# Kernel optimization log

Hardware: AMD Instinct MI355X
Metric: run time of the kernel (lower is better)

Reference implementation:

```python
import jax, jax.numpy as jnp
import numpy as np

D_MODEL = 2048
N_HEADS = 16
N_KV_HEADS = 4
HEAD_DIM = D_MODEL // N_HEADS  # 128
ROPE_DIM = 128
ROPE_BASE = 10000.0
B, T = 2, 8192


def setup_inputs() -> dict:
    key = jax.random.key(0)
    k1, k2, k3, k4 = jax.random.split(key, 4)
    s = 0.02
    return {
        "x": jax.random.normal(k1, (B, T, D_MODEL), dtype=jnp.float32),
        "wq": jax.random.normal(k2, (N_HEADS * HEAD_DIM, D_MODEL), dtype=jnp.float32) * s,
        "wk": jax.random.normal(k3, (N_KV_HEADS * HEAD_DIM, D_MODEL), dtype=jnp.float32) * s,
        "wv": jax.random.normal(k4, (N_KV_HEADS * HEAD_DIM, D_MODEL), dtype=jnp.float32) * s,
        "pos_offset": 0,
    }


def _shape_heads(y, n_heads):
    b, t, _ = y.shape
    # (B,T,H*D) -> (B,H,T,D)
    return y.reshape(b, t, n_heads, HEAD_DIM).transpose(0, 2, 1, 3)


def _rope(xh, pos_offset):
    # xh: (B,H,T,Dh); rotate first ROPE_DIM dims, llama-style rotate_half.
    t = xh.shape[2]
    half = ROPE_DIM // 2
    inv_freq = 1.0 / (ROPE_BASE ** (jnp.arange(0, ROPE_DIM, 2, dtype=jnp.float32) / ROPE_DIM))  # (half,)
    pos = jnp.arange(t, dtype=jnp.float32) + pos_offset  # (T,)
    freqs = pos[:, None] * inv_freq[None, :]  # (T, half)
    emb = jnp.concatenate([freqs, freqs], axis=-1)  # (T, ROPE_DIM)
    cos = jnp.cos(emb)[None, None]  # (1,1,T,ROPE_DIM)
    sin = jnp.sin(emb)[None, None]
    xr = xh[..., :ROPE_DIM]
    xp = xh[..., ROPE_DIM:]
    rot = jnp.concatenate([-xr[..., half:], xr[..., :half]], axis=-1)
    xr = xr * cos + rot * sin
    return jnp.concatenate([xr, xp], axis=-1) if xp.shape[-1] else xr


def reference(x, wq, wk, wv, pos_offset):
    # torch nn.Linear: y = x @ W.T
    q = jnp.einsum('btd,od->bto', x, wq)
    k = jnp.einsum('btd,od->bto', x, wk)
    v = jnp.einsum('btd,od->bto', x, wv)
    qh = _rope(_shape_heads(q, N_HEADS), pos_offset)    # (B,H,T,Dh)
    kh = _rope(_shape_heads(k, N_KV_HEADS), pos_offset)  # (B,Hkv,T,Dh)
    vh = _shape_heads(v, N_KV_HEADS)                     # (B,Hkv,T,Dh)
    return qh, kh, vh
```

## Files before the change

kernel.cpp:

```cpp
#include <hip/hip_runtime.h>
#include <hip/hip_bf16.h>


typedef __attribute__((ext_vector_type(8))) short short8;
typedef __attribute__((ext_vector_type(4))) float f32x4;

#define Q_BLOCK  33554432u
#define V_BASE   41943040u

__device__ __forceinline__ unsigned short f2bf(float f) {
  unsigned u = __float_as_uint(f);
  u += 0x7FFFu + ((u >> 16) & 1u);
  return (unsigned short)(u >> 16);
}
__device__ __forceinline__ float bf2f(unsigned short h) {
  return __uint_as_float(((unsigned)h) << 16);
}

__global__ void prep_kernel(const float* __restrict__ x,
                            const float* __restrict__ wq,
                            const float* __restrict__ wk,
                            const float* __restrict__ wv,
                            const int* __restrict__ pos_off,
                            unsigned short* __restrict__ Ahi,
                            unsigned short* __restrict__ Alo,
                            unsigned short* __restrict__ Bhi,
                            unsigned short* __restrict__ Blo,
                            float2* __restrict__ rt) {
  const int bid = blockIdx.x, t = threadIdx.x;
  if (bid < 2048) {
    int base = bid * 4096 + t;
    #pragma unroll
    for (int i = 0; i < 16; ++i) {
      int idx = base + i * 256;
      float4 v = ((const float4*)x)[idx];
      ushort4 h, l;
      h.x = f2bf(v.x); l.x = f2bf(v.x - bf2f(h.x));
      h.y = f2bf(v.y); l.y = f2bf(v.y - bf2f(h.y));
      h.z = f2bf(v.z); l.z = f2bf(v.z - bf2f(h.z));
      h.w = f2bf(v.w); l.w = f2bf(v.w - bf2f(h.w));
      ((ushort4*)Ahi)[idx] = h;
      ((ushort4*)Alo)[idx] = l;
    }
  } else if (bid < 2560) {
    int base = (bid - 2048) * 3072 + t;
    #pragma unroll
    for (int i = 0; i < 12; ++i) {
      int idx = base + i * 256;
      int n = idx >> 9, k4 = idx & 511;
      const float* src;
      if (n < 2048)      src = wq + (size_t)n * 2048;
      else if (n < 2560) src = wk + (size_t)(n - 2048) * 2048;
      else               src = wv + (size_t)(n - 2560) * 2048;
      float4 v = ((const float4*)src)[k4];
      ushort4 h, l;
      h.x = f2bf(v.x); l.x = f2bf(v.x - bf2f(h.x));
      h.y = f2bf(v.y); l.y = f2bf(v.y - bf2f(h.y));
      h.z = f2bf(v.z); l.z = f2bf(v.z - bf2f(h.z));
      h.w = f2bf(v.w); l.w = f2bf(v.w - bf2f(h.w));
      ((ushort4*)Bhi)[idx] = h;
      ((ushort4*)Blo)[idx] = l;
    }
  } else {
    __shared__ float sinv[64];
    if (t < 64) sinv[t] = (float)pow(10000.0, -(double)t / 64.0);
    __syncthreads();
    const int po = pos_off[0];
    int base = (bid - 2560) * 4096 + t;
    #pragma unroll
    for (int i = 0; i < 16; ++i) {
      int idx = base + i * 256;
      int trow = idx >> 6, j = idx & 63;
      float ang = (float)(trow + po) * sinv[j];
      double a = (double)ang;
      double k = rint(a * 0.15915494309189535);
      double r = a - k * 6.283185307179586;
      float rf = (float)r;
      rt[idx] = make_float2(cosf(rf), sinf(rf));
    }
  }
}

__global__ __launch_bounds__(512, 2) void gemm8_kernel(
    const unsigned short* __restrict__ Ahi, const unsigned short* __restrict__ Alo,
    const unsigned short* __restrict__ Bhi, const unsigned short* __restrict__ Blo,
    const float2* __restrict__ rt, float* __restrict__ out) {
  __shared__ __align__(16) unsigned short smem[65536];

  const int tid  = threadIdx.x;
  const int lane = tid & 63;
  const int wave = tid >> 6;
  const int wr   = wave >> 2;
  const int wc   = wave & 3;
  const int l15  = lane & 15, lk = lane >> 4;

  const int xcd = blockIdx.x & 7;
  const int loc = blockIdx.x >> 3;
  const int bm = xcd * 8 + loc / 12;
  const int bn = loc % 12;
  const int rowA = bm * 256;
  const int rowB = bn * 256;

  int grow[2], gk[2];
  #pragma unroll
  for (int L = 0; L < 2; ++L) {
    const int o = L * 4096 + tid * 8;
    const int lr = o >> 6;
    const int cs = (o >> 3) & 7;
    const int cl = cs ^ (lr & 7);
    grow[L] = lr + ((cl >> 2) << 7);
    gk[L]   = (cl & 3) << 3;
  }

  const int csA = ((wr << 2) + lk) ^ (l15 & 7);
  const int csB = (((wc >> 1) << 2) + lk) ^ (l15 & 7);

  f32x4 acc[8][4];
  #pragma unroll
  for (int m = 0; m < 8; ++m)
    #pragma unroll
    for (int n = 0; n < 4; ++n)
      acc[m][n] = (f32x4){0.f, 0.f, 0.f, 0.f};

  auto STAGE = [&](int n) {
    const unsigned short* As = (n < 128) ? Ahi : Alo;
    const unsigned short* Bs = (n < 64 || n >= 128) ? Bhi : Blo;
    const int kcol = (n & 63) << 5;
    const int sb = (n & 3) << 14;
    #pragma unroll
    for (int L = 0; L < 2; ++L) {
      const int o = L * 4096 + tid * 8;
      const unsigned short* ga = As + (size_t)(rowA + grow[L]) * 2048 + kcol + gk[L];
      __builtin_amdgcn_global_load_lds(
          (const __attribute__((address_space(1))) void*)ga,
          (__attribute__((address_space(3))) void*)&smem[sb + o], 16, 0, 0);
      const unsigned short* gb = Bs + (size_t)(rowB + grow[L]) * 2048 + kcol + gk[L];
      __builtin_amdgcn_global_load_lds(
          (const __attribute__((address_space(1))) void*)gb,
          (__attribute__((address_space(3))) void*)&smem[sb + 8192 + o], 16, 0, 0);
    }
  };

  STAGE(0); STAGE(1); STAGE(2);

  for (int j = 0; j < 192; ++j) {
    if (j) __builtin_amdgcn_s_barrier();
    if (j + 3 < 192) STAGE(j + 3);
    if (j < 189)       asm volatile("s_waitcnt vmcnt(12)" ::: "memory");
    else if (j == 189) asm volatile("s_waitcnt vmcnt(8)"  ::: "memory");
    else if (j == 190) asm volatile("s_waitcnt vmcnt(4)"  ::: "memory");
    else               asm volatile("s_waitcnt vmcnt(0)"  ::: "memory");
    __builtin_amdgcn_s_barrier();

    const int sb = (j & 3) << 14;
    short8 af[8], bf[4];
    #pragma unroll
    for (int mi = 0; mi < 8; ++mi)
      af[mi] = *(const short8*)&smem[sb + (mi * 16 + l15) * 64 + csA * 8];
    #pragma unroll
    for (int ni = 0; ni < 4; ++ni) {
      const int br = (wc & 1) * 32 + (ni & 1) * 16 + ((ni >> 1) << 6) + l15;
      bf[ni] = *(const short8*)&smem[sb + 8192 + br * 64 + csB * 8];
    }
    __builtin_amdgcn_s_setprio(1);
    #pragma unroll
    for (int mi = 0; mi < 8; ++mi)
      #pragma unroll
      for (int ni = 0; ni < 4; ++ni)
        acc[mi][ni] = __builtin_amdgcn_mfma_f32_16x16x32_bf16(
            af[mi], bf[ni], acc[mi][ni], 0, 0, 0);
    __builtin_amdgcn_s_setprio(0);
  }

  const int headglob = bn * 2 + (wc >> 1);
  size_t base; int nheads, head; bool dorope;
  if (headglob < 16)      { base = 0;       head = headglob;      nheads = 16; dorope = true; }
  else if (headglob < 20) { base = Q_BLOCK; head = headglob - 16; nheads = 4;  dorope = true; }
  else                    { base = V_BASE;  head = headglob - 20; nheads = 4;  dorope = false; }
  const int dbase = (wc & 1) * 32;

  #pragma unroll
  for (int m = 0; m < 8; ++m) {
    #pragma unroll
    for (int r = 0; r < 4; ++r) {
      const int row = bm * 256 + wr * 128 + m * 16 + lk * 4 + r;
      const int b = row >> 13, trow = row & 8191;
      float* op = out + base + (((size_t)(b * nheads + head) * 8192 + trow) << 7);
      #pragma unroll
      for (int n0 = 0; n0 < 2; ++n0) {
        const int d1 = dbase + n0 * 16 + l15;
        const float c1 = acc[m][n0][r];
        const float c2 = acc[m][n0 + 2][r];
        if (dorope) {
          const float2 cs = rt[(trow << 6) + d1];
          op[d1]      = c1 * cs.x - c2 * cs.y;
          op[d1 + 64] = c2 * cs.x + c1 * cs.y;
        } else {
          op[d1]      = c1;
          op[d1 + 64] = c2;
        }
      }
    }
  }
}

__global__ void fallback_kernel(const float* __restrict__ x,
                                const float* __restrict__ wq,
                                const float* __restrict__ wk,
                                const float* __restrict__ wv,
                                const int* __restrict__ pos_off,
                                float* __restrict__ out) {
  __shared__ float xs[2048];
  const int m = blockIdx.x;
  const int b = m >> 13, t = m & 8191;
  const float* xr = x + (size_t)m * 2048;
  for (int i = threadIdx.x; i < 2048; i += 256) xs[i] = xr[i];
  __syncthreads();

  const int n = blockIdx.y * 256 + threadIdx.x;
  const int d = n & 63;
  const float* w; size_t base; int head, nh; bool dorope;
  if (n < 1024)      { head = n >> 6;          w = wq + (size_t)(head * 128 + d) * 2048; base = 0;       nh = 16; dorope = true; }
  else if (n < 1280) { head = (n - 1024) >> 6; w = wk + (size_t)(head * 128 + d) * 2048; base = Q_BLOCK; nh = 4;  dorope = true; }
  else               { head = (n - 1280) >> 6; w = wv + (size_t)(head * 128 + d) * 2048; base = V_BASE;  nh = 4;  dorope = false; }

  const float* w2 = w + 64 * 2048;
  float c1 = 0.f, c2 = 0.f;
  for (int k = 0; k < 2048; ++k) { c1 += xs[k] * w[k]; c2 += xs[k] * w2[k]; }

  float* op = out + base + (((size_t)(b * nh + head) * 8192 + t) << 7);
  if (dorope) {
    double invf = pow(10000.0, -(double)d / 64.0);
    float ang = (float)(t + pos_off[0]) * (float)invf;
    float cs = (float)cos((double)ang), sn = (float)sin((double)ang);
    op[d]      = c1 * cs - c2 * sn;
    op[d + 64] = c2 * cs + c1 * sn;
  } else {
    op[d]      = c1;
    op[d + 64] = c2;
  }
}

extern "C" void kernel_launch(void* const* d_in, const int* in_sizes, int n_in,
                              void* d_out, int out_size, void* d_ws, size_t ws_size,
                              hipStream_t stream) {
  const float* x  = (const float*)d_in[0];
  const float* wq = (const float*)d_in[1];
  const float* wk = (const float*)d_in[2];
  const float* wv = (const float*)d_in[3];
  const int* pos  = (const int*)d_in[4];
  float* out = (float*)d_out;

  const size_t WS_NEEDED = 134217728ull + 25165824ull + 4194304ull;
  if (ws_size < WS_NEEDED) {
    fallback_kernel<<<dim3(16384, 6), 256, 0, stream>>>(x, wq, wk, wv, pos, out);
    return;
  }

  unsigned short* Ahi = (unsigned short*)d_ws;
  unsigned short* Alo = Ahi + 33554432;
  unsigned short* Bhi = Alo + 33554432;
  unsigned short* Blo = Bhi + 6291456;
  float2* rt = (float2*)(Blo + 6291456);

  prep_kernel<<<2688, 256, 0, stream>>>(x, wq, wk, wv, pos,
                                        Ahi, Alo, Bhi, Blo, rt);
  gemm8_kernel<<<768, 512, 0, stream>>>(Ahi, Alo, Bhi, Blo, rt, out);
}
```

Baseline: 922.0 us.

## Restructure GEMM mainloop into 8-wave ping-pong schedule with K=64 tiles

Replaces the 4-stage K=32 buffered loop with a double-buffered K=64 loop. Each iteration is split into four quadrant phases, each separated by barriers, and the global-to-LDS loads for the next tiles are interleaved between MFMA clusters. The LDS layout changes from a half-tile-swizzled K=32 arrangement to a plain 64-column XOR swizzle, with matching fragment offsets. The aim is to hide LDS read and global load latency behind MFMA work, at the cost of many more barriers per iteration and tighter vmcnt/lgkmcnt bookkeeping.

```diff
diff --git a/kernel.cpp b/kernel.cpp
--- a/kernel.cpp
+++ b/kernel.cpp
@@ -108,12 +108,12 @@
     const int lr = o >> 6;
     const int cs = (o >> 3) & 7;
     const int cl = cs ^ (lr & 7);
-    grow[L] = lr + ((cl >> 2) << 7);
-    gk[L]   = (cl & 3) << 3;
-  }
-
-  const int csA = ((wr << 2) + lk) ^ (l15 & 7);
-  const int csB = (((wc >> 1) << 2) + lk) ^ (l15 & 7);
+    grow[L] = lr;
+    gk[L]   = cl << 3;
+  }
+
+  const int ck0 = (((0 << 2) + lk) ^ (l15 & 7)) << 3;
+  const int ck1 = (((1 << 2) + lk) ^ (l15 & 7)) << 3;
 
   f32x4 acc[8][4];
   #pragma unroll
@@ -122,54 +122,123 @@
     for (int n = 0; n < 4; ++n)
       acc[m][n] = (f32x4){0.f, 0.f, 0.f, 0.f};
 
-  auto STAGE = [&](int n) {
-    const unsigned short* As = (n < 128) ? Ahi : Alo;
-    const unsigned short* Bs = (n < 64 || n >= 128) ? Bhi : Blo;
-    const int kcol = (n & 63) << 5;
-    const int sb = (n & 3) << 14;
+  auto Asel = [&](int tt) { return (tt < 64) ? Ahi : Alo; };
+  auto Bsel = [&](int tt) { return (tt < 32 || tt >= 64) ? Bhi : Blo; };
+
+  auto STAGE = [&](int dst, const unsigned short* src, int rowbase, int kc) {
     #pragma unroll
     for (int L = 0; L < 2; ++L) {
       const int o = L * 4096 + tid * 8;
-      const unsigned short* ga = As + (size_t)(rowA + grow[L]) * 2048 + kcol + gk[L];
+      const unsigned short* g = src + (size_t)(rowbase + grow[L]) * 2048 + kc + gk[L];
       __builtin_amdgcn_global_load_lds(
-          (const __attribute__((address_space(1))) void*)ga,
-          (__attribute__((address_space(3))) void*)&smem[sb + o], 16, 0, 0);
-      const unsigned short* gb = Bs + (size_t)(rowB + grow[L]) * 2048 + kcol + gk[L];
-      __builtin_amdgcn_global_load_lds(
-          (const __attribute__((address_space(1))) void*)gb,
-          (__attribute__((address_space(3))) void*)&smem[sb + 8192 + o], 16, 0, 0);
+          (const __attribute__((address_space(1))) void*)g,
+          (__attribute__((address_space(3))) void*)&smem[dst + o], 16, 0, 0);
     }
   };
 
-  STAGE(0); STAGE(1); STAGE(2);
-
-  for (int j = 0; j < 192; ++j) {
-    if (j) __builtin_amdgcn_s_barrier();
-    if (j + 3 < 192) STAGE(j + 3);
-    if (j < 189)       asm volatile("s_waitcnt vmcnt(12)" ::: "memory");
-    else if (j == 189) asm volatile("s_waitcnt vmcnt(8)"  ::: "memory");
-    else if (j == 190) asm volatile("s_waitcnt vmcnt(4)"  ::: "memory");
-    else               asm volatile("s_waitcnt vmcnt(0)"  ::: "memory");
-    __builtin_amdgcn_s_barrier();
-
-    const int sb = (j & 3) << 14;
-    short8 af[8], bf[4];
-    #pragma unroll
-    for (int mi = 0; mi < 8; ++mi)
-      af[mi] = *(const short8*)&smem[sb + (mi * 16 + l15) * 64 + csA * 8];
-    #pragma unroll
-    for (int ni = 0; ni < 4; ++ni) {
-      const int br = (wc & 1) * 32 + (ni & 1) * 16 + ((ni >> 1) << 6) + l15;
-      bf[ni] = *(const short8*)&smem[sb + 8192 + br * 64 + csB * 8];
-    }
+  STAGE(0 + 16384,     Bhi, rowB,       0);
+  STAGE(0 + 24576,     Bhi, rowB + 128, 0);
+  STAGE(0 + 0,         Ahi, rowA,       0);
+  STAGE(0 + 8192,      Ahi, rowA + 128, 0);
+  STAGE(32768 + 16384, Bhi, rowB,       64);
+  STAGE(32768 + 24576, Bhi, rowB + 128, 64);
+  asm volatile("s_waitcnt vmcnt(4)" ::: "memory");
+  __builtin_amdgcn_s_barrier();
+
+  short8 afA[4][2], bf0[2][2], bf1[2][2];
+
+  for (int t = 0; t < 96; ++t) {
+    const int cb  = (t & 1) << 15;
+    const int ob  = cb ^ 32768;
+    const int aoff = cb + wr * 8192;
+    const int boff = cb + 16384 + (wc >> 1) * 8192;
+    const int brow0 = (wc & 1) * 32;
+
+    #pragma unroll
+    for (int mi = 0; mi < 4; ++mi) {
+      const int r = mi * 16 + l15;
+      afA[mi][0] = *(const short8*)&smem[aoff + r * 64 + ck0];
+      afA[mi][1] = *(const short8*)&smem[aoff + r * 64 + ck1];
+    }
+    #pragma unroll
+    for (int ni = 0; ni < 2; ++ni) {
+      const int r = brow0 + ni * 16 + l15;
+      bf0[ni][0] = *(const short8*)&smem[boff + r * 64 + ck0];
+      bf0[ni][1] = *(const short8*)&smem[boff + r * 64 + ck1];
+    }
+    if (t < 95) STAGE(ob + 0, Asel(t + 1), rowA, ((t + 1) & 31) << 6);
+    asm volatile("s_waitcnt lgkmcnt(8)" ::: "memory");
+    __builtin_amdgcn_s_barrier();
+    asm volatile("s_waitcnt lgkmcnt(0)" ::: "memory");
     __builtin_amdgcn_s_setprio(1);
     #pragma unroll
-    for (int mi = 0; mi < 8; ++mi)
-      #pragma unroll
-      for (int ni = 0; ni < 4; ++ni)
-        acc[mi][ni] = __builtin_amdgcn_mfma_f32_16x16x32_bf16(
-            af[mi], bf[ni], acc[mi][ni], 0, 0, 0);
+    for (int mi = 0; mi < 4; ++mi)
+      #pragma unroll
+      for (int ni = 0; ni < 2; ++ni)
+        #pragma unroll
+        for (int kk = 0; kk < 2; ++kk)
+          acc[mi][ni] = __builtin_amdgcn_mfma_f32_16x16x32_bf16(
+              afA[mi][kk], bf0[ni][kk], acc[mi][ni], 0, 0, 0);
     __builtin_amdgcn_s_setprio(0);
+    __builtin_amdgcn_s_barrier();
+
+    #pragma unroll
+    for (int ni = 0; ni < 2; ++ni) {
+      const int r = brow0 + 64 + ni * 16 + l15;
+      bf1[ni][0] = *(const short8*)&smem[boff + r * 64 + ck0];
+      bf1[ni][1] = *(const short8*)&smem[boff + r * 64 + ck1];
+    }
+    if (t < 95) STAGE(ob + 8192, Asel(t + 1), rowA + 128, ((t + 1) & 31) << 6);
+    __builtin_amdgcn_s_barrier();
+    asm volatile("s_waitcnt lgkmcnt(0)" ::: "memory");
+    __builtin_amdgcn_s_setprio(1);
+    #pragma unroll
+    for (int mi = 0; mi < 4; ++mi)
+      #pragma unroll
+      for (int ni = 0; ni < 2; ++ni)
+        #pragma unroll
+        for (int kk = 0; kk < 2; ++kk)
+          acc[mi][2 + ni] = __builtin_amdgcn_mfma_f32_16x16x32_bf16(
+              afA[mi][kk], bf1[ni][kk], acc[mi][2 + ni], 0, 0, 0);
+    __builtin_amdgcn_s_setprio(0);
+    __builtin_amdgcn_s_barrier();
+
+    #pragma unroll
+    for (int mi = 0; mi < 4; ++mi) {
+      const int r = 64 + mi * 16 + l15;
+      afA[mi][0] = *(const short8*)&smem[aoff + r * 64 + ck0];
+      afA[mi][1] = *(const short8*)&smem[aoff + r * 64 + ck1];
+    }
+    if (t < 94) STAGE(cb + 16384, Bsel(t + 2), rowB, ((t + 2) & 31) << 6);
+    __builtin_amdgcn_s_barrier();
+    asm volatile("s_waitcnt lgkmcnt(0)" ::: "memory");
+    __builtin_amdgcn_s_setprio(1);
+    #pragma unroll
+    for (int mi = 0; mi < 4; ++mi)
+      #pragma unroll
+      for (int ni = 0; ni < 2; ++ni)
+        #pragma unroll
+        for (int kk = 0; kk < 2; ++kk)
+          acc[4 + mi][ni] = __builtin_amdgcn_mfma_f32_16x16x32_bf16(
+              afA[mi][kk], bf0[ni][kk], acc[4 + mi][ni], 0, 0, 0);
+    __builtin_amdgcn_s_setprio(0);
+    __builtin_amdgcn_s_barrier();
+
+    if (t < 94) STAGE(cb + 24576, Bsel(t + 2), rowB + 128, ((t + 2) & 31) << 6);
+    if (t < 94)       asm volatile("s_waitcnt vmcnt(4)" ::: "memory");
+    else if (t == 94) asm volatile("s_waitcnt vmcnt(0)" ::: "memory");
+    __builtin_amdgcn_s_barrier();
+    __builtin_amdgcn_s_setprio(1);
+    #pragma unroll
+    for (int mi = 0; mi < 4; ++mi)
+      #pragma unroll
+      for (int ni = 0; ni < 2; ++ni)
+        #pragma unroll
+        for (int kk = 0; kk < 2; ++kk)
+          acc[4 + mi][2 + ni] = __builtin_amdgcn_mfma_f32_16x16x32_bf16(
+              afA[mi][kk], bf1[ni][kk], acc[4 + mi][2 + ni], 0, 0, 0);
+    __builtin_amdgcn_s_setprio(0);
+    __builtin_amdgcn_s_barrier();
   }
 
   const int headglob = bn * 2 + (wc >> 1);
```

Result: faster. 847.8 us (-8.1%).
